# Optimization experiments

Hardware: AMD Instinct MI355X
Metric: run time of the kernel (lower is better)

## Reference

```python
import jax, jax.numpy as jnp
import numpy as np

EMBED = 1024
HEADS = 16
HEAD_DIM = EMBED // HEADS


def setup_inputs() -> dict:
    key = jax.random.key(0)
    ks = jax.random.split(key, 6)
    B, S = 4, 2048
    scale = 1.0 / np.sqrt(EMBED)
    x = jax.random.normal(ks[0], (B, S, EMBED), dtype=jnp.float32)
    Wq = jax.random.normal(ks[1], (EMBED, EMBED), dtype=jnp.float32) * scale
    Wk = jax.random.normal(ks[2], (EMBED, EMBED), dtype=jnp.float32) * scale
    Wv = jax.random.normal(ks[3], (EMBED, EMBED), dtype=jnp.float32) * scale
    Wo = jax.random.normal(ks[4], (EMBED, EMBED), dtype=jnp.float32) * scale
    bo = jnp.zeros((EMBED,), dtype=jnp.float32)
    return {"x": x, "Wq": Wq, "Wk": Wk, "Wv": Wv, "Wo": Wo, "bo": bo}


def reference(x, Wq, Wk, Wv, Wo, bo):
    B, S, E = x.shape
    H, D = HEADS, HEAD_DIM
    # nn.Linear(no bias): y = x @ W.T ; then split heads -> [B,H,S,D]
    q = (x @ Wq.T).reshape(B, S, H, D).transpose(0, 2, 1, 3)
    k = (x @ Wk.T).reshape(B, S, H, D).transpose(0, 2, 1, 3)
    v = (x @ Wv.T).reshape(B, S, H, D).transpose(0, 2, 1, 3)
    # scores [B,H,S,S] with causal mask (tril)
    energy = jnp.einsum('bhqd,bhkd->bhqk', q, k) / jnp.sqrt(jnp.float32(D))
    causal = jnp.tril(jnp.ones((S, S), dtype=bool))
    energy = jnp.where(causal[None, None], energy, jnp.float32(-jnp.inf))
    attn = jax.nn.softmax(energy, axis=-1)
    # dropout is identity in eval / p used here = 0.0
    out = jnp.einsum('bhqk,bhkd->bhqd', attn, v)
    out = out.transpose(0, 2, 1, 3).reshape(B, S, E)
    return out @ Wo.T + bo
```

## Files before the change

kernel.cpp:

```cpp
#include <hip/hip_runtime.h>
#include <math.h>

#define EMBED 1024
#define HEADS 16
#define HDIM  64
#define SEQ   2048
#define BATCH 4
#define QBLK  128
#define KVBLK 128
#define NQT   (SEQ / QBLK)
#define QSCALE 0.18033688011112042f

typedef __attribute__((ext_vector_type(8))) short short8;
typedef __attribute__((ext_vector_type(4))) float f32x4;
typedef __attribute__((ext_vector_type(16))) float f32x16;
typedef __attribute__((ext_vector_type(2))) unsigned int uint2v;

__device__ __forceinline__ unsigned short f2b(float f) {
    union { float f; unsigned int u; } c; c.f = f;
    unsigned int r = (c.u + 0x7fffu + ((c.u >> 16) & 1u)) >> 16;
    return (unsigned short)r;
}

__device__ __forceinline__ unsigned int cvtpk(float lo, float hi) {
    unsigned int r;
    asm("v_cvt_pk_bf16_f32 %0, %1, %2" : "=v"(r) : "v"(lo), "v"(hi));
    return r;
}

__device__ __forceinline__ void gld16(const void* g, void* l) {
    __builtin_amdgcn_global_load_lds((__attribute__((address_space(1))) void*)g,
                                     (__attribute__((address_space(3))) void*)l,
                                     16, 0, 0);
}

__device__ __forceinline__ f32x16 zero16() {
    f32x16 z;
#pragma unroll
    for (int i = 0; i < 16; ++i) z[i] = 0.f;
    return z;
}

__device__ __forceinline__ void makePB(const f32x16 s, short8& f0, short8& f1) {
    union { unsigned int u[4]; short8 s8; } t;
    {
        unsigned int A0 = cvtpk(s[0], s[1]), A1 = cvtpk(s[2], s[3]);
        unsigned int B0 = cvtpk(s[4], s[5]), B1 = cvtpk(s[6], s[7]);
        uint2v w0 = __builtin_amdgcn_permlane32_swap(A0, B0, false, false);
        uint2v w1 = __builtin_amdgcn_permlane32_swap(A1, B1, false, false);
        t.u[0] = w0[0]; t.u[1] = w1[0]; t.u[2] = w0[1]; t.u[3] = w1[1];
        f0 = t.s8;
    }
    {
        unsigned int A0 = cvtpk(s[8], s[9]), A1 = cvtpk(s[10], s[11]);
        unsigned int B0 = cvtpk(s[12], s[13]), B1 = cvtpk(s[14], s[15]);
        uint2v w0 = __builtin_amdgcn_permlane32_swap(A0, B0, false, false);
        uint2v w1 = __builtin_amdgcn_permlane32_swap(A1, B1, false, false);
        t.u[0] = w0[0]; t.u[1] = w1[0]; t.u[2] = w0[1]; t.u[3] = w1[1];
        f1 = t.s8;
    }
}

__global__ __launch_bounds__(256) void cast_bf16(const float* __restrict__ src,
                                                 unsigned short* __restrict__ dst,
                                                 int n) {
    int i = (blockIdx.x * 256 + threadIdx.x) * 8;
    if (i >= n) return;
    float4 a = *(const float4*)(src + i);
    float4 b = *(const float4*)(src + i + 4);
    short8 v;
    v[0] = (short)f2b(a.x); v[1] = (short)f2b(a.y);
    v[2] = (short)f2b(a.z); v[3] = (short)f2b(a.w);
    v[4] = (short)f2b(b.x); v[5] = (short)f2b(b.y);
    v[6] = (short)f2b(b.z); v[7] = (short)f2b(b.w);
    *(short8*)(dst + i) = v;
}

template <int MODE>
__global__ __launch_bounds__(256) void gemm_bf16(const unsigned short* __restrict__ A,
                                                 const unsigned short* __restrict__ W,
                                                 void* __restrict__ outp,
                                                 const float* __restrict__ bias) {
    const int K_ = EMBED;
    __shared__ __attribute__((aligned(16))) unsigned short As[128 * 32];
    __shared__ __attribute__((aligned(16))) unsigned short Bs[128 * 32];

    const int tid  = threadIdx.x;
    const int lane = tid & 63;
    const int w    = tid >> 6;
    const int wr   = w >> 1, wc = w & 1;
    const int m0 = blockIdx.y * 128, n0 = blockIdx.x * 128;

    const unsigned short* gA = A + (size_t)(m0 + w * 32 + (lane >> 2)) * K_ + (lane & 3) * 8;
    const unsigned short* gB = W + (size_t)(n0 + w * 32 + (lane >> 2)) * K_ + (lane & 3) * 8;
    unsigned short* lA = As + (w * 32) * 32;
    unsigned short* lB = Bs + (w * 32) * 32;

    f32x4 zero = {0.f, 0.f, 0.f, 0.f};
    f32x4 acc[4][4];
#pragma unroll
    for (int i = 0; i < 4; ++i)
#pragma unroll
        for (int j = 0; j < 4; ++j) acc[i][j] = zero;

    for (int k0 = 0; k0 < K_; k0 += 32) {
        gld16(gA, lA);
        gld16(gA + (size_t)16 * K_, lA + 16 * 32);
        gld16(gB, lB);
        gld16(gB + (size_t)16 * K_, lB + 16 * 32);
        gA += 32; gB += 32;
        __syncthreads();
        short8 af[4], bfr[4];
#pragma unroll
        for (int i = 0; i < 4; ++i) {
            af[i]  = *(const short8*)&As[(wr * 64 + i * 16 + (lane & 15)) * 32 + (lane >> 4) * 8];
            bfr[i] = *(const short8*)&Bs[(wc * 64 + i * 16 + (lane & 15)) * 32 + (lane >> 4) * 8];
        }
#pragma unroll
        for (int i = 0; i < 4; ++i)
#pragma unroll
            for (int j = 0; j < 4; ++j)
                acc[i][j] = __builtin_amdgcn_mfma_f32_16x16x32_bf16(af[i], bfr[j], acc[i][j], 0, 0, 0);
        __syncthreads();
    }

    if (MODE == 0) {
        const size_t PP = (size_t)BATCH * SEQ * EMBED;
        unsigned short* dst = (unsigned short*)outp;
#pragma unroll
        for (int i = 0; i < 4; ++i)
#pragma unroll
            for (int ni = 0; ni < 4; ++ni) {
                int n = n0 + wc * 64 + ni * 16 + (lane & 15);
                int which = n >> 10;
                int h = (n >> 6) & 15, d = n & 63;
                float os = (which == 0) ? QSCALE : 1.0f;
#pragma unroll
                for (int j = 0; j < 4; ++j) {
                    int m = m0 + wr * 64 + i * 16 + (lane >> 4) * 4 + j;
                    int b = m >> 11, s = m & (SEQ - 1);
                    dst[(size_t)which * PP + (((size_t)b * HEADS + h) * SEQ + s) * HDIM + d] =
                        f2b(acc[i][ni][j] * os);
                }
            }
    } else {
        float* dst = (float*)outp;
#pragma unroll
        for (int i = 0; i < 4; ++i)
#pragma unroll
            for (int ni = 0; ni < 4; ++ni) {
                int n = n0 + wc * 64 + ni * 16 + (lane & 15);
                float bv = bias[n];
#pragma unroll
                for (int j = 0; j < 4; ++j) {
                    int m = m0 + wr * 64 + i * 16 + (lane >> 4) * 4 + j;
                    dst[(size_t)m * EMBED + n] = acc[i][ni][j] + bv;
                }
            }
    }
}

__global__ __launch_bounds__(256, 2) void attn_mfma32(const unsigned short* __restrict__ Q,
                                                      const unsigned short* __restrict__ K,
                                                      const unsigned short* __restrict__ V,
                                                      unsigned short* __restrict__ att) {
    __shared__ __attribute__((aligned(16))) unsigned short KsL[2][KVBLK * 64];
    __shared__ __attribute__((aligned(16))) unsigned short VtL[2][64 * KVBLK];

    const int tid  = threadIdx.x;
    const int lane = tid & 63;
    const int wv   = tid >> 6;
    const int hi   = lane >> 5;
    const int lq   = lane & 31;
    const int bh   = blockIdx.y;
    const int qtA  = (NQT - 1) - blockIdx.x;
    const int qtB  = blockIdx.x;
    const size_t base = (size_t)bh * SEQ * HDIM;

    const int krow = tid >> 3;
    const int kxor = ((tid & 7) ^ (krow & 7)) * 8;
    const int vkp = tid & 63, vo = (tid >> 6) * 2;

    const int ksw = (lq & 7) << 4;

    short8 qf[4];
    auto loadQ = [&](int qt) {
        const unsigned short* qrow =
            Q + base + (size_t)(qt * QBLK + wv * 32 + lq) * HDIM + hi * 8;
        qf[0] = *(const short8*)(qrow);
        qf[1] = *(const short8*)(qrow + 16);
        qf[2] = *(const short8*)(qrow + 32);
        qf[3] = *(const short8*)(qrow + 48);
    };

    auto stageK = [&](int k0, int bufi) {
        const unsigned short* g0 = K + base + (size_t)(k0 + krow) * HDIM + kxor;
        unsigned short* l0 = &KsL[bufi][wv * 512];
#pragma unroll
        for (int j = 0; j < 4; ++j)
            gld16(g0 + (size_t)(32 * j) * HDIM, l0 + j * 2048);
    };

    short8 va0, vb0, va1, vb1;
    auto loadV = [&](int k0) {
        const unsigned short* vp = V + base + (size_t)(k0 + 2 * vkp) * HDIM;
        va0 = *(const short8*)(vp + vo * 8);
        vb0 = *(const short8*)(vp + HDIM + vo * 8);
        va1 = *(const short8*)(vp + (vo + 1) * 8);
        vb1 = *(const short8*)(vp + HDIM + (vo + 1) * 8);
    };
    auto writeV = [&](int bufi) {
        char* vb_ = (char*)&VtL[bufi][0];
#pragma unroll
        for (int e = 0; e < 8; ++e) {
            unsigned int p0 = (unsigned int)(unsigned short)va0[e] |
                              ((unsigned int)(unsigned short)vb0[e] << 16);
            *(unsigned int*)(vb_ + ((vo * 8 + e) << 8) + ((4 * vkp) ^ (e << 4))) = p0;
            unsigned int p1 = (unsigned int)(unsigned short)va1[e] |
                              ((unsigned int)(unsigned short)vb1[e] << 16);
            *(unsigned int*)(vb_ + (((vo + 1) * 8 + e) << 8) + ((4 * vkp) ^ (e << 4))) = p1;
        }
    };

    f32x16 o0 = zero16(), o1 = zero16();
    float m_run = -INFINITY, l_run = 0.f;

    const int b_ = bh >> 4, h_ = bh & 15;
    auto writeOut = [&](int q0w_) {
        const float invl = 1.f / l_run;
        unsigned short* orow =
            att + ((size_t)b_ * SEQ + (q0w_ + lq)) * EMBED + h_ * HDIM + 4 * hi;
#pragma unroll
        for (int c = 0; c < 4; ++c) {
            unsigned int w0 = cvtpk(o0[4 * c] * invl, o0[4 * c + 1] * invl);
            unsigned int w1 = cvtpk(o0[4 * c + 2] * invl, o0[4 * c + 3] * invl);
            *(uint2*)(orow + 8 * c) = make_uint2(w0, w1);
            unsigned int w2 = cvtpk(o1[4 * c] * invl, o1[4 * c + 1] * invl);
            unsigned int w3 = cvtpk(o1[4 * c + 2] * invl, o1[4 * c + 3] * invl);
            *(uint2*)(orow + 32 + 8 * c) = make_uint2(w2, w3);
        }
    };

    loadQ(qtA);
    int qtCur = qtA;
    int q0w = qtA * QBLK + wv * 32;
    int qsel = q0w + lq;
    stageK(0, 0);
    loadV(0);
    writeV(0);
    __syncthreads();

    const int niter = NQT + 1;
    for (int i = 0; i < niter; ++i) {
        const int buf = i & 1, nbuf = buf ^ 1;
        const int kt = (i <= qtA) ? i : (i - qtA - 1);
        const int k0 = kt * KVBLK;
        const bool pf = (i + 1 < niter);

        if (pf) {
            const int ktN = (i + 1 <= qtA) ? (i + 1) : (i - qtA);
            const int k0N = ktN * KVBLK;
            stageK(k0N, nbuf);
            loadV(k0N);
        }

        const char* kbase = (const char*)&KsL[buf][0];
        f32x16 sS[4];
        __builtin_amdgcn_s_setprio(1);
#pragma unroll
        for (int c = 0; c < 4; ++c) {
            const char* kb_ = kbase + ((c * 32 + lq) << 7);
            f32x16 acc = zero16();
#pragma unroll
            for (int dc = 0; dc < 4; ++dc) {
                short8 kf = *(const short8*)(kb_ + ((((dc << 1) | hi) << 4) ^ ksw));
                acc = __builtin_amdgcn_mfma_f32_32x32x16_bf16(kf, qf[dc], acc, 0, 0, 0);
            }
            sS[c] = acc;
        }
        __builtin_amdgcn_s_setprio(0);

        if (kt == qtCur) {
#pragma unroll
            for (int c = 0; c < 4; ++c)
#pragma unroll
                for (int r = 0; r < 16; ++r) {
                    int key = k0 + 32 * c + (r & 3) + 8 * (r >> 2) + 4 * hi;
                    if (key > qsel) sS[c][r] = -INFINITY;
                }
        }

        f32x16 t;
#pragma unroll
        for (int r = 0; r < 16; ++r)
            t[r] = fmaxf(fmaxf(sS[0][r], sS[1][r]), fmaxf(sS[2][r], sS[3][r]));
        float m8[8];
#pragma unroll
        for (int r = 0; r < 8; ++r) m8[r] = fmaxf(t[r], t[r + 8]);
        float m4[4];
#pragma unroll
        for (int r = 0; r < 4; ++r) m4[r] = fmaxf(m8[r], m8[r + 4]);
        float mx = fmaxf(fmaxf(m4[0], m4[1]), fmaxf(m4[2], m4[3]));
        mx = fmaxf(mx, __shfl_xor(mx, 32));

        if (__any(mx > m_run + 8.0f)) {
            float mnew = fmaxf(m_run, mx);
            float scl = __builtin_exp2f(m_run - mnew);
            m_run = mnew;
            l_run *= scl;
#pragma unroll
            for (int r = 0; r < 16; ++r) { o0[r] *= scl; o1[r] *= scl; }
        }

#pragma unroll
        for (int c = 0; c < 4; ++c)
#pragma unroll
            for (int r = 0; r < 16; ++r)
                sS[c][r] = __builtin_exp2f(sS[c][r] - m_run);

        f32x16 u;
#pragma unroll
        for (int r = 0; r < 16; ++r)
            u[r] = (sS[0][r] + sS[1][r]) + (sS[2][r] + sS[3][r]);
        float s8[8];
#pragma unroll
        for (int r = 0; r < 8; ++r) s8[r] = u[r] + u[r + 8];
        float s4[4];
#pragma unroll
        for (int r = 0; r < 4; ++r) s4[r] = s8[r] + s8[r + 4];
        float ps = (s4[0] + s4[1]) + (s4[2] + s4[3]);
        ps += __shfl_xor(ps, 32);
        l_run += ps;

        const char* vtb = (const char*)&VtL[buf][0];
        __builtin_amdgcn_s_setprio(1);
#pragma unroll
        for (int c = 0; c < 4; ++c) {
            short8 pb0, pb1;
            makePB(sS[c], pb0, pb1);
            short8 vf;
            vf = *(const short8*)(vtb + (lq << 8) + ((c * 64 + hi * 16) ^ ksw));
            o0 = __builtin_amdgcn_mfma_f32_32x32x16_bf16(vf, pb0, o0, 0, 0, 0);
            vf = *(const short8*)(vtb + (lq << 8) + ((c * 64 + 32 + hi * 16) ^ ksw));
            o0 = __builtin_amdgcn_mfma_f32_32x32x16_bf16(vf, pb1, o0, 0, 0, 0);
            vf = *(const short8*)(vtb + ((32 + lq) << 8) + ((c * 64 + hi * 16) ^ ksw));
            o1 = __builtin_amdgcn_mfma_f32_32x32x16_bf16(vf, pb0, o1, 0, 0, 0);
            vf = *(const short8*)(vtb + ((32 + lq) << 8) + ((c * 64 + 32 + hi * 16) ^ ksw));
            o1 = __builtin_amdgcn_mfma_f32_32x32x16_bf16(vf, pb1, o1, 0, 0, 0);
        }
        __builtin_amdgcn_s_setprio(0);

        if (pf) writeV(nbuf);
        __syncthreads();

        if (i == qtA) {
            writeOut(q0w);
            o0 = zero16(); o1 = zero16();
            m_run = -INFINITY; l_run = 0.f;
            loadQ(qtB);
            qtCur = qtB;
            q0w = qtB * QBLK + wv * 32;
            qsel = q0w + lq;
        }
    }
    writeOut(q0w);
}

extern "C" void kernel_launch(void* const* d_in, const int* in_sizes, int n_in,
                              void* d_out, int out_size, void* d_ws, size_t ws_size,
                              hipStream_t stream) {
    const float* x  = (const float*)d_in[0];
    const float* Wq = (const float*)d_in[1];
    const float* Wk = (const float*)d_in[2];
    const float* Wv = (const float*)d_in[3];
    const float* Wo = (const float*)d_in[4];
    const float* bo = (const float*)d_in[5];

    const size_t XN = (size_t)BATCH * SEQ * EMBED;
    const size_t WN = (size_t)EMBED * EMBED;

    unsigned short* ws   = (unsigned short*)d_ws;
    unsigned short* xb   = ws;
    unsigned short* wqkv = xb + XN;
    unsigned short* wob  = wqkv + 3 * WN;
    unsigned short* Qb   = wob + WN;
    unsigned short* attb = Qb + 3 * XN;

    cast_bf16<<<(int)(XN / 2048), 256, 0, stream>>>(x, xb, (int)XN);
    cast_bf16<<<(int)(WN / 2048), 256, 0, stream>>>(Wq, wqkv, (int)WN);
    cast_bf16<<<(int)(WN / 2048), 256, 0, stream>>>(Wk, wqkv + WN, (int)WN);
    cast_bf16<<<(int)(WN / 2048), 256, 0, stream>>>(Wv, wqkv + 2 * WN, (int)WN);
    cast_bf16<<<(int)(WN / 2048), 256, 0, stream>>>(Wo, wob, (int)WN);

    gemm_bf16<0><<<dim3(3 * EMBED / 128, BATCH * SEQ / 128), 256, 0, stream>>>(
        xb, wqkv, Qb, nullptr);

    attn_mfma32<<<dim3(NQT / 2, BATCH * HEADS), 256, 0, stream>>>(
        Qb, Qb + XN, Qb + 2 * XN, attb);

    gemm_bf16<1><<<dim3(EMBED / 128, BATCH * SEQ / 128), 256, 0, stream>>>(
        attb, wob, d_out, bo);
}
```

Baseline: 194.9 us.

## Merge cast kernels, remap GEMM blocks for XCDs, split attention per q-tile with diagonal skipping

```diff
diff --git a/kernel.cpp b/kernel.cpp
--- a/kernel.cpp
+++ b/kernel.cpp
@@ -61,18 +61,32 @@
     }
 }
 
-__global__ __launch_bounds__(256) void cast_bf16(const float* __restrict__ src,
-                                                 unsigned short* __restrict__ dst,
-                                                 int n) {
-    int i = (blockIdx.x * 256 + threadIdx.x) * 8;
-    if (i >= n) return;
+__global__ __launch_bounds__(256) void cast_all(const float* __restrict__ x,
+                                                const float* __restrict__ wq,
+                                                const float* __restrict__ wk,
+                                                const float* __restrict__ wv,
+                                                const float* __restrict__ wo,
+                                                unsigned short* __restrict__ xb,
+                                                unsigned short* __restrict__ wqkv,
+                                                unsigned short* __restrict__ wob) {
+    const int WNblk = 512;
+    int b = blockIdx.x;
+    const float* src;
+    unsigned short* dst;
+    int off;
+    if (b < 4096)            { src = x;  dst = xb;                    off = b; }
+    else if (b < 4096 + WNblk)   { src = wq; dst = wqkv;              off = b - 4096; }
+    else if (b < 4096 + 2*WNblk) { src = wk; dst = wqkv + 1024*1024;  off = b - 4096 - WNblk; }
+    else if (b < 4096 + 3*WNblk) { src = wv; dst = wqkv + 2*1024*1024; off = b - 4096 - 2*WNblk; }
+    else                     { src = wo; dst = wob;                   off = b - 4096 - 3*WNblk; }
+    int i = (off * 256 + threadIdx.x) * 8;
     float4 a = *(const float4*)(src + i);
-    float4 b = *(const float4*)(src + i + 4);
+    float4 c = *(const float4*)(src + i + 4);
     short8 v;
     v[0] = (short)f2b(a.x); v[1] = (short)f2b(a.y);
     v[2] = (short)f2b(a.z); v[3] = (short)f2b(a.w);
-    v[4] = (short)f2b(b.x); v[5] = (short)f2b(b.y);
-    v[6] = (short)f2b(b.z); v[7] = (short)f2b(b.w);
+    v[4] = (short)f2b(c.x); v[5] = (short)f2b(c.y);
+    v[6] = (short)f2b(c.z); v[7] = (short)f2b(c.w);
     *(short8*)(dst + i) = v;
 }
 
@@ -89,7 +103,11 @@
     const int lane = tid & 63;
     const int w    = tid >> 6;
     const int wr   = w >> 1, wc = w & 1;
-    const int m0 = blockIdx.y * 128, n0 = blockIdx.x * 128;
+
+    const int nbx = (MODE == 0) ? 24 : 8;
+    const int cpx = (MODE == 0) ? 192 : 64;
+    const int nb  = (blockIdx.x & 7) * cpx + (blockIdx.x >> 3);
+    const int m0 = (nb / nbx) * 128, n0 = (nb % nbx) * 128;
 
     const unsigned short* gA = A + (size_t)(m0 + w * 32 + (lane >> 2)) * K_ + (lane & 3) * 8;
     const unsigned short* gB = W + (size_t)(n0 + w * 32 + (lane >> 2)) * K_ + (lane & 3) * 8;
@@ -160,38 +178,35 @@
     }
 }
 
-__global__ __launch_bounds__(256, 2) void attn_mfma32(const unsigned short* __restrict__ Q,
+__global__ __launch_bounds__(256, 3) void attn_mfma32(const unsigned short* __restrict__ Q,
                                                       const unsigned short* __restrict__ K,
                                                       const unsigned short* __restrict__ V,
                                                       unsigned short* __restrict__ att) {
     __shared__ __attribute__((aligned(16))) unsigned short KsL[2][KVBLK * 64];
-    __shared__ __attribute__((aligned(16))) unsigned short VtL[2][64 * KVBLK];
+    __shared__ __attribute__((aligned(16))) unsigned short VtL[64 * KVBLK];
 
     const int tid  = threadIdx.x;
     const int lane = tid & 63;
     const int wv   = tid >> 6;
     const int hi   = lane >> 5;
     const int lq   = lane & 31;
-    const int bh   = blockIdx.y;
-    const int qtA  = (NQT - 1) - blockIdx.x;
-    const int qtB  = blockIdx.x;
+    const int bid  = blockIdx.x;
+    const int qt   = (NQT - 1) - (bid >> 6);
+    const int bh   = (bid & 7) * 8 + ((bid >> 3) & 7);
     const size_t base = (size_t)bh * SEQ * HDIM;
 
     const int krow = tid >> 3;
     const int kxor = ((tid & 7) ^ (krow & 7)) * 8;
     const int vkp = tid & 63, vo = (tid >> 6) * 2;
-
     const int ksw = (lq & 7) << 4;
 
+    const unsigned short* qrow =
+        Q + base + (size_t)(qt * QBLK + wv * 32 + lq) * HDIM + hi * 8;
     short8 qf[4];
-    auto loadQ = [&](int qt) {
-        const unsigned short* qrow =
-            Q + base + (size_t)(qt * QBLK + wv * 32 + lq) * HDIM + hi * 8;
-        qf[0] = *(const short8*)(qrow);
-        qf[1] = *(const short8*)(qrow + 16);
-        qf[2] = *(const short8*)(qrow + 32);
-        qf[3] = *(const short8*)(qrow + 48);
-    };
+    qf[0] = *(const short8*)(qrow);
+    qf[1] = *(const short8*)(qrow + 16);
+    qf[2] = *(const short8*)(qrow + 32);
+    qf[3] = *(const short8*)(qrow + 48);
 
     auto stageK = [&](int k0, int bufi) {
         const unsigned short* g0 = K + base + (size_t)(k0 + krow) * HDIM + kxor;
@@ -209,8 +224,8 @@
         va1 = *(const short8*)(vp + (vo + 1) * 8);
         vb1 = *(const short8*)(vp + HDIM + (vo + 1) * 8);
     };
-    auto writeV = [&](int bufi) {
-        char* vb_ = (char*)&VtL[bufi][0];
+    auto writeV = [&]() {
+        char* vb_ = (char*)&VtL[0];
 #pragma unroll
         for (int e = 0; e < 8; ++e) {
             unsigned int p0 = (unsigned int)(unsigned short)va0[e] |
@@ -225,75 +240,67 @@
     f32x16 o0 = zero16(), o1 = zero16();
     float m_run = -INFINITY, l_run = 0.f;
 
-    const int b_ = bh >> 4, h_ = bh & 15;
-    auto writeOut = [&](int q0w_) {
-        const float invl = 1.f / l_run;
-        unsigned short* orow =
-            att + ((size_t)b_ * SEQ + (q0w_ + lq)) * EMBED + h_ * HDIM + 4 * hi;
-#pragma unroll
-        for (int c = 0; c < 4; ++c) {
-            unsigned int w0 = cvtpk(o0[4 * c] * invl, o0[4 * c + 1] * invl);
-            unsigned int w1 = cvtpk(o0[4 * c + 2] * invl, o0[4 * c + 3] * invl);
-            *(uint2*)(orow + 8 * c) = make_uint2(w0, w1);
-            unsigned int w2 = cvtpk(o1[4 * c] * invl, o1[4 * c + 1] * invl);
-            unsigned int w3 = cvtpk(o1[4 * c + 2] * invl, o1[4 * c + 3] * invl);
-            *(uint2*)(orow + 32 + 8 * c) = make_uint2(w2, w3);
-        }
-    };
-
-    loadQ(qtA);
-    int qtCur = qtA;
-    int q0w = qtA * QBLK + wv * 32;
-    int qsel = q0w + lq;
+    const int q0w  = qt * QBLK + wv * 32;
+    const int qsel = q0w + lq;
+
     stageK(0, 0);
     loadV(0);
-    writeV(0);
+    writeV();
     __syncthreads();
 
-    const int niter = NQT + 1;
-    for (int i = 0; i < niter; ++i) {
-        const int buf = i & 1, nbuf = buf ^ 1;
-        const int kt = (i <= qtA) ? i : (i - qtA - 1);
+    for (int kt = 0; kt <= qt; ++kt) {
+        const int buf = kt & 1;
         const int k0 = kt * KVBLK;
-        const bool pf = (i + 1 < niter);
+        const bool pf = (kt < qt);
 
         if (pf) {
-            const int ktN = (i + 1 <= qtA) ? (i + 1) : (i - qtA);
-            const int k0N = ktN * KVBLK;
-            stageK(k0N, nbuf);
-            loadV(k0N);
+            stageK(k0 + KVBLK, buf ^ 1);
+            loadV(k0 + KVBLK);
         }
 
         const char* kbase = (const char*)&KsL[buf][0];
+        const char* vtb   = (const char*)&VtL[0];
+        const bool diag = (kt == qt);
+        const int cmax = diag ? wv : 3;
+
         f32x16 sS[4];
         __builtin_amdgcn_s_setprio(1);
 #pragma unroll
         for (int c = 0; c < 4; ++c) {
-            const char* kb_ = kbase + ((c * 32 + lq) << 7);
-            f32x16 acc = zero16();
-#pragma unroll
-            for (int dc = 0; dc < 4; ++dc) {
-                short8 kf = *(const short8*)(kb_ + ((((dc << 1) | hi) << 4) ^ ksw));
-                acc = __builtin_amdgcn_mfma_f32_32x32x16_bf16(kf, qf[dc], acc, 0, 0, 0);
-            }
-            sS[c] = acc;
+            if (c <= cmax) {
+                const char* kb_ = kbase + ((c * 32 + lq) << 7);
+                f32x16 acc = zero16();
+#pragma unroll
+                for (int dc = 0; dc < 4; ++dc) {
+                    short8 kf = *(const short8*)(kb_ + ((((dc << 1) | hi) << 4) ^ ksw));
+                    acc = __builtin_amdgcn_mfma_f32_32x32x16_bf16(kf, qf[dc], acc, 0, 0, 0);
+                }
+                sS[c] = acc;
+            }
         }
         __builtin_amdgcn_s_setprio(0);
 
-        if (kt == qtCur) {
-#pragma unroll
-            for (int c = 0; c < 4; ++c)
-#pragma unroll
-                for (int r = 0; r < 16; ++r) {
-                    int key = k0 + 32 * c + (r & 3) + 8 * (r >> 2) + 4 * hi;
-                    if (key > qsel) sS[c][r] = -INFINITY;
+        if (diag) {
+#pragma unroll
+            for (int c = 0; c < 4; ++c) {
+                if (c == wv) {
+#pragma unroll
+                    for (int r = 0; r < 16; ++r) {
+                        int key = k0 + 32 * c + (r & 3) + 8 * (r >> 2) + 4 * hi;
+                        if (key > qsel) sS[c][r] = -INFINITY;
+                    }
                 }
-        }
-
-        f32x16 t;
-#pragma unroll
-        for (int r = 0; r < 16; ++r)
-            t[r] = fmaxf(fmaxf(sS[0][r], sS[1][r]), fmaxf(sS[2][r], sS[3][r]));
+            }
+        }
+
+        f32x16 t = sS[0];
+#pragma unroll
+        for (int c = 1; c < 4; ++c) {
+            if (c <= cmax) {
+#pragma unroll
+                for (int r = 0; r < 16; ++r) t[r] = fmaxf(t[r], sS[c][r]);
+            }
+        }
         float m8[8];
 #pragma unroll
         for (int r = 0; r < 8; ++r) m8[r] = fmaxf(t[r], t[r + 8]);
@@ -313,15 +320,22 @@
         }
 
 #pragma unroll
-        for (int c = 0; c < 4; ++c)
-#pragma unroll
-            for (int r = 0; r < 16; ++r)
-                sS[c][r] = __builtin_exp2f(sS[c][r] - m_run);
-
-        f32x16 u;
-#pragma unroll
-        for (int r = 0; r < 16; ++r)
-            u[r] = (sS[0][r] + sS[1][r]) + (sS[2][r] + sS[3][r]);
+        for (int c = 0; c < 4; ++c) {
+            if (c <= cmax) {
+#pragma unroll
+                for (int r = 0; r < 16; ++r)
+                    sS[c][r] = __builtin_exp2f(sS[c][r] - m_run);
+            }
+        }
+
+        f32x16 u = sS[0];
+#pragma unroll
+        for (int c = 1; c < 4; ++c) {
+            if (c <= cmax) {
+#pragma unroll
+                for (int r = 0; r < 16; ++r) u[r] += sS[c][r];
+            }
+        }
         float s8[8];
 #pragma unroll
         for (int r = 0; r < 8; ++r) s8[r] = u[r] + u[r + 8];
@@ -332,38 +346,45 @@
         ps += __shfl_xor(ps, 32);
         l_run += ps;
 
-        const char* vtb = (const char*)&VtL[buf][0];
         __builtin_amdgcn_s_setprio(1);
 #pragma unroll
         for (int c = 0; c < 4; ++c) {
-            short8 pb0, pb1;
-            makePB(sS[c], pb0, pb1);
-            short8 vf;
-            vf = *(const short8*)(vtb + (lq << 8) + ((c * 64 + hi * 16) ^ ksw));
-            o0 = __builtin_amdgcn_mfma_f32_32x32x16_bf16(vf, pb0, o0, 0, 0, 0);
-            vf = *(const short8*)(vtb + (lq << 8) + ((c * 64 + 32 + hi * 16) ^ ksw));
-            o0 = __builtin_amdgcn_mfma_f32_32x32x16_bf16(vf, pb1, o0, 0, 0, 0);
-            vf = *(const short8*)(vtb + ((32 + lq) << 8) + ((c * 64 + hi * 16) ^ ksw));
-            o1 = __builtin_amdgcn_mfma_f32_32x32x16_bf16(vf, pb0, o1, 0, 0, 0);
-            vf = *(const short8*)(vtb + ((32 + lq) << 8) + ((c * 64 + 32 + hi * 16) ^ ksw));
-            o1 = __builtin_amdgcn_mfma_f32_32x32x16_bf16(vf, pb1, o1, 0, 0, 0);
+            if (c <= cmax) {
+                short8 pb0, pb1;
+                makePB(sS[c], pb0, pb1);
+                short8 vf;
+                vf = *(const short8*)(vtb + (lq << 8) + ((c * 64 + hi * 16) ^ ksw));
+                o0 = __builtin_amdgcn_mfma_f32_32x32x16_bf16(vf, pb0, o0, 0, 0, 0);
+                vf = *(const short8*)(vtb + (lq << 8) + ((c * 64 + 32 + hi * 16) ^ ksw));
+                o0 = __builtin_amdgcn_mfma_f32_32x32x16_bf16(vf, pb1, o0, 0, 0, 0);
+                vf = *(const short8*)(vtb + ((32 + lq) << 8) + ((c * 64 + hi * 16) ^ ksw));
+                o1 = __builtin_amdgcn_mfma_f32_32x32x16_bf16(vf, pb0, o1, 0, 0, 0);
+                vf = *(const short8*)(vtb + ((32 + lq) << 8) + ((c * 64 + 32 + hi * 16) ^ ksw));
+                o1 = __builtin_amdgcn_mfma_f32_32x32x16_bf16(vf, pb1, o1, 0, 0, 0);
+            }
         }
         __builtin_amdgcn_s_setprio(0);
 
-        if (pf) writeV(nbuf);
         __syncthreads();
-
-        if (i == qtA) {
-            writeOut(q0w);
-            o0 = zero16(); o1 = zero16();
-            m_run = -INFINITY; l_run = 0.f;
-            loadQ(qtB);
-            qtCur = qtB;
-            q0w = qtB * QBLK + wv * 32;
-            qsel = q0w + lq;
-        }
-    }
-    writeOut(q0w);
+        if (pf) {
+            writeV();
+            __syncthreads();
+        }
+    }
+
+    const int b_ = bh >> 4, h_ = bh & 15;
+    const float invl = 1.f / l_run;
+    unsigned short* orow =
+        att + ((size_t)b_ * SEQ + (q0w + lq)) * EMBED + h_ * HDIM + 4 * hi;
+#pragma unroll
+    for (int c = 0; c < 4; ++c) {
+        unsigned int w0 = cvtpk(o0[4 * c] * invl, o0[4 * c + 1] * invl);
+        unsigned int w1 = cvtpk(o0[4 * c + 2] * invl, o0[4 * c + 3] * invl);
+        *(uint2*)(orow + 8 * c) = make_uint2(w0, w1);
+        unsigned int w2 = cvtpk(o1[4 * c] * invl, o1[4 * c + 1] * invl);
+        unsigned int w3 = cvtpk(o1[4 * c + 2] * invl, o1[4 * c + 3] * invl);
+        *(uint2*)(orow + 32 + 8 * c) = make_uint2(w2, w3);
+    }
 }
 
 extern "C" void kernel_launch(void* const* d_in, const int* in_sizes, int n_in,
@@ -386,18 +407,12 @@
     unsigned short* Qb   = wob + WN;
     unsigned short* attb = Qb + 3 * XN;
 
-    cast_bf16<<<(int)(XN / 2048), 256, 0, stream>>>(x, xb, (int)XN);
-    cast_bf16<<<(int)(WN / 2048), 256, 0, stream>>>(Wq, wqkv, (int)WN);
-    cast_bf16<<<(int)(WN / 2048), 256, 0, stream>>>(Wk, wqkv + WN, (int)WN);
-    cast_bf16<<<(int)(WN / 2048), 256, 0, stream>>>(Wv, wqkv + 2 * WN, (int)WN);
-    cast_bf16<<<(int)(WN / 2048), 256, 0, stream>>>(Wo, wob, (int)WN);
-
-    gemm_bf16<0><<<dim3(3 * EMBED / 128, BATCH * SEQ / 128), 256, 0, stream>>>(
-        xb, wqkv, Qb, nullptr);
-
-    attn_mfma32<<<dim3(NQT / 2, BATCH * HEADS), 256, 0, stream>>>(
+    cast_all<<<4096 + 4 * 512, 256, 0, stream>>>(x, Wq, Wk, Wv, Wo, xb, wqkv, wob);
+
+    gemm_bf16<0><<<1536, 256, 0, stream>>>(xb, wqkv, Qb, nullptr);
+
+    attn_mfma32<<<NQT * BATCH * HEADS, 256, 0, stream>>>(
         Qb, Qb + XN, Qb + 2 * XN, attb);
 
-    gemm_bf16<1><<<dim3(EMBED / 128, BATCH * SEQ / 128), 256, 0, stream>>>(
-        attb, wob, d_out, bo);
-}
+    gemm_bf16<1><<<512, 256, 0, stream>>>(attb, wob, d_out, bo);
+}
```

Measured after the change: 227.2 us. 16.6% more time.
